# Kernel tuning notes

Measured on AMD Instinct MI355X. Metric: run time of the kernel, lower is better.

Reference implementation:

```python
import jax, jax.numpy as jnp
import numpy as np

N_NODES = 100_000
E_OFF = 1_500_000
LATENT = 64
MP_STEPS = 3


def setup_inputs() -> dict:
    key = jax.random.key(0)
    ks = jax.random.split(key, 12)
    # lower-triangular graph: all self-loops + random off-diagonal edges with row >= col
    r = jax.random.randint(ks[0], (E_OFF,), 0, N_NODES)
    c = jax.random.randint(ks[1], (E_OFF,), 0, N_NODES)
    diag = jnp.arange(N_NODES)
    edge_row = jnp.concatenate([jnp.maximum(r, c), diag]).astype(jnp.int64)
    edge_col = jnp.concatenate([jnp.minimum(r, c), diag]).astype(jnp.int64)
    E = E_OFF + N_NODES
    # positive weights (gcn_norm takes deg^{-1/2} of weighted degree)
    edge_attr = jax.random.uniform(ks[2], (E,), jnp.float32) + 0.05
    x = jax.random.normal(ks[3], (N_NODES, 1), jnp.float32)
    L = LATENT
    def lin(k, fi, fo):
        return jax.random.normal(k, (fi, fo), jnp.float32) / np.sqrt(fi)
    return {
        "x": x,
        "edge_attr": edge_attr,
        "w_enc": lin(ks[4], 1, L), "b_enc": jnp.zeros((L,), jnp.float32),
        "conv1_w": jax.random.normal(ks[5], (MP_STEPS, L, L), jnp.float32) / np.sqrt(L),
        "conv1_b": jnp.zeros((MP_STEPS, L), jnp.float32),
        "conv2_w": jax.random.normal(ks[6], (MP_STEPS, L, L), jnp.float32) / np.sqrt(L),
        "conv2_b": jnp.zeros((MP_STEPS, L), jnp.float32),
        "dec_w1": lin(ks[7], 2 * L, L), "dec_b1": jnp.zeros((L,), jnp.float32),
        "dec_w2": lin(ks[8], L, 1), "dec_b2": jnp.zeros((1,), jnp.float32),
        "edge_row": edge_row,
        "edge_col": edge_col,
    }


def reference(x, edge_attr, w_enc, b_enc, conv1_w, conv1_b, conv2_w, conv2_b,
              dec_w1, dec_b1, dec_w2, dec_b2, edge_row, edge_col):
    N = x.shape[0]
    # GCN normalization (graph already contains all self-loops, so PyG's
    # add_remaining_self_loops is a no-op and keeps existing loop weights)
    deg = jax.ops.segment_sum(edge_attr, edge_col, num_segments=N)
    dinv = jnp.where(deg > 0, jax.lax.rsqrt(jnp.maximum(deg, 1e-30)), 0.0)
    norm = dinv[edge_row] * edge_attr * dinv[edge_col]  # [E]
    cnt = jnp.maximum(
        jax.ops.segment_sum(jnp.ones_like(edge_attr), edge_col, num_segments=N), 1.0
    )[:, None]  # mean aggregation denominator

    def gcn(h, W, b):
        m = (h @ W)[edge_row] * norm[:, None]           # [E, F] messages
        agg = jax.ops.segment_sum(m, edge_col, num_segments=N) / cnt
        return agg + b

    # node encoder: single Linear (no activation)
    h = x @ w_enc + b_enc
    for i in range(MP_STEPS):
        h = jax.nn.relu(gcn(h, conv1_w[i], conv1_b[i]))
        h = jax.nn.relu(gcn(h, conv2_w[i], conv2_b[i]))

    # edge decoder: gather endpoints, MLP [2L -> L -> 1]
    e = jnp.concatenate([h[edge_row], h[edge_col]], axis=1)
    e = jax.nn.relu(e @ dec_w1 + dec_b1)
    e = (e @ dec_w2 + dec_b2)[:, 0]                      # [E]
    vals = jnp.where(edge_row == edge_col, jax.nn.softplus(e), e)
    return vals
```

## Files before the change

kernel.cpp:

```cpp
#include <hip/hip_runtime.h>
#include <hip/hip_fp16.h>
#include <math.h>

#define L 64
#define FIXS 1048576.0f
#define WAITCNT_LGKM0 0xC07F

static __device__ __forceinline__ __half2 h2add(__half2 a, __half2 b) {
    return __half2{__hadd(a.x, b.x), __hadd(a.y, b.y)};
}
static __device__ __forceinline__ __half2 h2relu(__half2 a) {
    const __half z = __float2half(0.f);
    return __half2{__hgt(a.x, z) ? a.x : z, __hgt(a.y, z) ? a.y : z};
}


__global__ void k_hist(const int* __restrict__ col, const float* __restrict__ attr,
                       unsigned long long* __restrict__ degcnt,
                       int* __restrict__ rank, int E) {
    int e = blockIdx.x * blockDim.x + threadIdx.x;
    if (e < E) {
        int c = col[e];
        unsigned int fx = (unsigned int)(int)rintf(attr[e] * FIXS);
        unsigned long long old = atomicAdd(&degcnt[c], (1ULL << 32) | (unsigned long long)fx);
        rank[e] = (int)(old >> 32);
    }
}

__global__ void k_dinv(const unsigned long long* __restrict__ degcnt,
                       float* __restrict__ dinv, int* __restrict__ cntI,
                       float* __restrict__ rcnt, int N) {
    int n = blockIdx.x * blockDim.x + threadIdx.x;
    if (n < N) {
        unsigned long long p = degcnt[n];
        int cnt = (int)(p >> 32);
        float d = (float)(unsigned int)(p & 0xffffffffULL) * (1.0f / FIXS);
        dinv[n] = (d > 0.f) ? (1.0f / sqrtf(fmaxf(d, 1e-30f))) : 0.f;
        cntI[n] = cnt;
        int c = cnt; if (c < 1) c = 1;
        rcnt[n] = 1.0f / (float)c;
    }
}


__global__ __launch_bounds__(256) void k_scan_a(const int* __restrict__ cntI,
                                                int* __restrict__ blockSums, int N) {
    __shared__ int red[4];
    int b = blockIdx.x, t = threadIdx.x;
    int base = b * 1024 + t * 4;
    int s = 0;
    #pragma unroll
    for (int i = 0; i < 4; ++i) { int idx = base + i; if (idx < N) s += cntI[idx]; }
    #pragma unroll
    for (int off = 32; off > 0; off >>= 1) s += __shfl_down(s, off);
    if ((t & 63) == 0) red[t >> 6] = s;
    __syncthreads();
    if (t == 0) blockSums[b] = red[0] + red[1] + red[2] + red[3];
}

__global__ __launch_bounds__(1024) void k_scan_b(int* __restrict__ blockSums, int B,
                                                 int* __restrict__ ptr, int N) {
    __shared__ int sh[1024];
    int t = threadIdx.x;
    sh[t] = (t < B) ? blockSums[t] : 0;
    __syncthreads();
    for (int off = 1; off < 1024; off <<= 1) {
        int v = (t >= off) ? sh[t - off] : 0;
        __syncthreads();
        sh[t] += v;
        __syncthreads();
    }
    if (t < B) blockSums[t] = (t == 0) ? 0 : sh[t - 1];
    if (t == B - 1) ptr[N] = sh[t];
}

__global__ __launch_bounds__(256) void k_scan_c(const int* __restrict__ cntI,
                                                const int* __restrict__ blockSums,
                                                int* __restrict__ ptr, int N) {
    __shared__ int th[256];
    int b = blockIdx.x, t = threadIdx.x;
    int base = b * 1024 + t * 4;
    int v[4]; int s = 0;
    #pragma unroll
    for (int i = 0; i < 4; ++i) {
        int idx = base + i;
        v[i] = (idx < N) ? cntI[idx] : 0;
        s += v[i];
    }
    th[t] = s;
    __syncthreads();
    for (int off = 1; off < 256; off <<= 1) {
        int x = (t >= off) ? th[t - off] : 0;
        __syncthreads();
        th[t] += x;
        __syncthreads();
    }
    int pre = ((t == 0) ? 0 : th[t - 1]) + blockSums[b];
    #pragma unroll
    for (int i = 0; i < 4; ++i) {
        int idx = base + i;
        if (idx < N) ptr[idx] = pre;
        pre += v[i];
    }
}

__global__ void k_scatter(const int* __restrict__ row, const int* __restrict__ col,
                          const float* __restrict__ attr, const float* __restrict__ dinv,
                          const int* __restrict__ colptr, const int* __restrict__ rank,
                          unsigned* __restrict__ csrX, int E) {
    int e = blockIdx.x * blockDim.x + threadIdx.x;
    if (e < E) {
        int r = row[e], c = col[e];
        float nrm = dinv[r] * attr[e] * dinv[c];
        unsigned short nb = __half_as_ushort(__float2half(nrm));
        csrX[colptr[c] + rank[e]] = (unsigned)r | ((unsigned)nb << 17);
    }
}


__global__ void k_encode(const float* __restrict__ x, const float* __restrict__ w_enc,
                         const float* __restrict__ b_enc, __half* __restrict__ h, int N) {
    int idx = blockIdx.x * blockDim.x + threadIdx.x;
    if (idx < N * L) {
        int n = idx >> 6, f = idx & 63;
        h[idx] = __float2half(x[n] * w_enc[f] + b_enc[f]);
    }
}


__global__ __launch_bounds__(256) void k_gcn(const uint2* __restrict__ h_in2,
        __half* __restrict__ h_out,
        const float* __restrict__ W, const float* __restrict__ bias,
        const int* __restrict__ colptr, const unsigned* __restrict__ csrX,
        const float* __restrict__ rcnt, int N) {
    __shared__ float sm[4][72];
    int lane = threadIdx.x & 63;
    int warp = threadIdx.x >> 6;
    int grp  = lane >> 4;
    int sub  = lane & 15;
    int wid  = (blockIdx.x * blockDim.x + threadIdx.x) >> 6;
    int nw   = (gridDim.x * blockDim.x) >> 6;
    float* smw = &sm[warp][0];

    float Wc[L];
    #pragma unroll
    for (int f = 0; f < L; ++f) Wc[f] = W[f * L + lane];
    float bl = bias[lane];

    for (int n = wid; n < N; n += nw) {
        int beg = colptr[n], end = colptr[n + 1];
        float4 sA = make_float4(0.f, 0.f, 0.f, 0.f);
        float4 sB = make_float4(0.f, 0.f, 0.f, 0.f);
        float4 sC = make_float4(0.f, 0.f, 0.f, 0.f);
        float4 sD = make_float4(0.f, 0.f, 0.f, 0.f);
        for (int base = beg; base < end; base += 64) {
            int m = end - base; if (m > 64) m = 64;
            unsigned mw = 0;
            if (lane < m) mw = csrX[base + lane];
            int kmax = (m + 3) >> 2;
            int k = 0;
            for (; k + 4 <= kmax; k += 4) {
                int j0 = 4 * k + grp;
                unsigned x0 = (unsigned)__shfl((int)mw, j0);
                unsigned x1 = (unsigned)__shfl((int)mw, j0 + 4);
                unsigned x2 = (unsigned)__shfl((int)mw, j0 + 8);
                unsigned x3 = (unsigned)__shfl((int)mw, j0 + 12);
                int r0 = (int)(x0 & 0x1FFFFu), r1 = (int)(x1 & 0x1FFFFu);
                int r2 = (int)(x2 & 0x1FFFFu), r3 = (int)(x3 & 0x1FFFFu);
                float w0 = __half2float(__ushort_as_half((unsigned short)(x0 >> 17)));
                float w1 = __half2float(__ushort_as_half((unsigned short)(x1 >> 17)));
                float w2 = __half2float(__ushort_as_half((unsigned short)(x2 >> 17)));
                float w3 = __half2float(__ushort_as_half((unsigned short)(x3 >> 17)));
                uint2 q0 = h_in2[(size_t)r0 * 16 + sub];
                uint2 q1 = h_in2[(size_t)r1 * 16 + sub];
                uint2 q2 = h_in2[(size_t)r2 * 16 + sub];
                uint2 q3 = h_in2[(size_t)r3 * 16 + sub];
                float2 l0 = __half22float2(*(__half2*)&q0.x), g0 = __half22float2(*(__half2*)&q0.y);
                float2 l1 = __half22float2(*(__half2*)&q1.x), g1 = __half22float2(*(__half2*)&q1.y);
                float2 l2 = __half22float2(*(__half2*)&q2.x), g2 = __half22float2(*(__half2*)&q2.y);
                float2 l3 = __half22float2(*(__half2*)&q3.x), g3 = __half22float2(*(__half2*)&q3.y);
                sA.x += w0 * l0.x; sA.y += w0 * l0.y; sA.z += w0 * g0.x; sA.w += w0 * g0.y;
                sB.x += w1 * l1.x; sB.y += w1 * l1.y; sB.z += w1 * g1.x; sB.w += w1 * g1.y;
                sC.x += w2 * l2.x; sC.y += w2 * l2.y; sC.z += w2 * g2.x; sC.w += w2 * g2.y;
                sD.x += w3 * l3.x; sD.y += w3 * l3.y; sD.z += w3 * g3.x; sD.w += w3 * g3.y;
            }
            for (; k < kmax; ++k) {
                int j0 = 4 * k + grp;
                unsigned x0 = (unsigned)__shfl((int)mw, j0);
                int   r0 = (int)(x0 & 0x1FFFFu);
                float w0 = __half2float(__ushort_as_half((unsigned short)(x0 >> 17)));
                uint2 q0 = h_in2[(size_t)r0 * 16 + sub];
                float2 l0 = __half22float2(*(__half2*)&q0.x), g0 = __half22float2(*(__half2*)&q0.y);
                sA.x += w0 * l0.x; sA.y += w0 * l0.y; sA.z += w0 * g0.x; sA.w += w0 * g0.y;
            }
        }
        float4 s;
        s.x = (sA.x + sB.x) + (sC.x + sD.x);
        s.y = (sA.y + sB.y) + (sC.y + sD.y);
        s.z = (sA.z + sB.z) + (sC.z + sD.z);
        s.w = (sA.w + sB.w) + (sC.w + sD.w);
        s.x += __shfl_xor(s.x, 16); s.x += __shfl_xor(s.x, 32);
        s.y += __shfl_xor(s.y, 16); s.y += __shfl_xor(s.y, 32);
        s.z += __shfl_xor(s.z, 16); s.z += __shfl_xor(s.z, 32);
        s.w += __shfl_xor(s.w, 16); s.w += __shfl_xor(s.w, 32);
        if (grp == 0) {
            smw[4 * sub + 0] = s.x; smw[4 * sub + 1] = s.y;
            smw[4 * sub + 2] = s.z; smw[4 * sub + 3] = s.w;
        }
        __builtin_amdgcn_s_waitcnt(WAITCNT_LGKM0);
        float a0 = 0.f, a1 = 0.f, a2 = 0.f, a3 = 0.f;
        const float4* smv = (const float4*)smw;
        #pragma unroll
        for (int q = 0; q < 16; ++q) {
            float4 sv = smv[q];
            a0 += sv.x * Wc[4 * q + 0];
            a1 += sv.y * Wc[4 * q + 1];
            a2 += sv.z * Wc[4 * q + 2];
            a3 += sv.w * Wc[4 * q + 3];
        }
        float o = ((a0 + a1) + (a2 + a3)) * rcnt[n] + bl;
        h_out[(size_t)n * L + lane] = __float2half(fmaxf(o, 0.f));
    }
}


__global__ __launch_bounds__(256) void k_mv2(const __half* __restrict__ h,
        const float* __restrict__ W1, const float* __restrict__ b1,
        __half* __restrict__ U, __half* __restrict__ V, int N) {
    __shared__ float sm[4][72];
    int lane = threadIdx.x & 63;
    int warp = threadIdx.x >> 6;
    int wid  = (blockIdx.x * blockDim.x + threadIdx.x) >> 6;
    int nw   = (gridDim.x * blockDim.x) >> 6;
    float* smw = &sm[warp][0];
    float Wu[L], Wv[L];
    #pragma unroll
    for (int f = 0; f < L; ++f) Wu[f] = W1[f * L + lane];
    #pragma unroll
    for (int f = 0; f < L; ++f) Wv[f] = W1[(L + f) * L + lane];
    float bl = b1[lane];
    for (int n = wid; n < N; n += nw) {
        float hl = __half2float(h[(size_t)n * L + lane]);
        smw[lane] = hl;
        __builtin_amdgcn_s_waitcnt(WAITCNT_LGKM0);
        float a0 = 0.f, a1 = 0.f, c0 = 0.f, c1 = 0.f;
        const float4* smv = (const float4*)smw;
        #pragma unroll
        for (int q = 0; q < 16; ++q) {
            float4 sv = smv[q];
            a0 += sv.x * Wu[4 * q + 0] ; a1 += sv.y * Wu[4 * q + 1];
            a0 += sv.z * Wu[4 * q + 2] ; a1 += sv.w * Wu[4 * q + 3];
            c0 += sv.x * Wv[4 * q + 0] ; c1 += sv.y * Wv[4 * q + 1];
            c0 += sv.z * Wv[4 * q + 2] ; c1 += sv.w * Wv[4 * q + 3];
        }
        U[(size_t)n * L + lane] = __float2half((a0 + a1) + bl);
        V[(size_t)n * L + lane] = __float2half(c0 + c1);
        __builtin_amdgcn_s_waitcnt(WAITCNT_LGKM0);
    }
}


__global__ __launch_bounds__(256) void k_edge(const __half* __restrict__ U,
        const __half* __restrict__ V, const float* __restrict__ w2,
        const float* __restrict__ b2,
        const int* __restrict__ colptr, const unsigned* __restrict__ csrX,
        float* __restrict__ tmp, int N) {
    int lane = threadIdx.x & 63;
    int half = lane & 1;
    int wid  = (blockIdx.x * blockDim.x + threadIdx.x) >> 6;
    int nw   = (gridDim.x * blockDim.x) >> 6;
    float w2f[32];
    #pragma unroll
    for (int k = 0; k < 32; ++k) w2f[k] = w2[32 * half + k];
    float b2v = b2[0];

    for (int n = wid; n < N; n += nw) {
        int beg = colptr[n], end = colptr[n + 1];
        const uint4* vrow = (const uint4*)(V + (size_t)n * L + 32 * half);
        uint4 v0 = vrow[0], v1 = vrow[1], v2 = vrow[2], v3 = vrow[3];
        for (int base = beg; base < end; base += 32) {
            int epos = base + (lane >> 1);
            if (epos < end) {
                unsigned md = csrX[epos];
                int r = (int)(md & 0x1FFFFu);
                const uint4* urow = (const uint4*)(U + (size_t)r * L + 32 * half);
                uint4 u0 = urow[0], u1 = urow[1], u2 = urow[2], u3 = urow[3];
                float p = 0.f;
                #define DOT8(uq, vq, B) { \
                    __half2 ta = h2relu(h2add(*(__half2*)&(uq).x, *(__half2*)&(vq).x)); \
                    __half2 tb = h2relu(h2add(*(__half2*)&(uq).y, *(__half2*)&(vq).y)); \
                    __half2 tc = h2relu(h2add(*(__half2*)&(uq).z, *(__half2*)&(vq).z)); \
                    __half2 td = h2relu(h2add(*(__half2*)&(uq).w, *(__half2*)&(vq).w)); \
                    float2 fa = __half22float2(ta), fb = __half22float2(tb); \
                    float2 fc = __half22float2(tc), fd = __half22float2(td); \
                    p += fa.x * w2f[B+0] + fa.y * w2f[B+1] + fb.x * w2f[B+2] + fb.y * w2f[B+3]; \
                    p += fc.x * w2f[B+4] + fc.y * w2f[B+5] + fd.x * w2f[B+6] + fd.y * w2f[B+7]; }
                DOT8(u0, v0, 0) DOT8(u1, v1, 8) DOT8(u2, v2, 16) DOT8(u3, v3, 24)
                #undef DOT8
                p += __shfl_xor(p, 1);
                if (half == 0) {
                    float val = p + b2v;
                    if (r == n) val = fmaxf(val, 0.f) + log1pf(expf(-fabsf(val)));
                    tmp[epos] = val;
                }
            }
        }
    }
}


__global__ void k_perm(const int* __restrict__ ecol, const int* __restrict__ rank,
                       const int* __restrict__ colptr, const float* __restrict__ tmp,
                       float* __restrict__ out, int E) {
    int e = blockIdx.x * blockDim.x + threadIdx.x;
    if (e < E) out[e] = tmp[colptr[ecol[e]] + rank[e]];
}


extern "C" void kernel_launch(void* const* d_in, const int* in_sizes, int n_in,
                              void* d_out, int out_size, void* d_ws, size_t ws_size,
                              hipStream_t stream) {
    const float* x     = (const float*)d_in[0];
    const float* attr  = (const float*)d_in[1];
    const float* w_enc = (const float*)d_in[2];
    const float* b_enc = (const float*)d_in[3];
    const float* c1w   = (const float*)d_in[4];
    const float* c1b   = (const float*)d_in[5];
    const float* c2w   = (const float*)d_in[6];
    const float* c2b   = (const float*)d_in[7];
    const float* dw1   = (const float*)d_in[8];
    const float* db1   = (const float*)d_in[9];
    const float* dw2   = (const float*)d_in[10];
    const float* db2   = (const float*)d_in[11];
    const int*   erow  = (const int*)d_in[12];
    const int*   ecol  = (const int*)d_in[13];
    int N = in_sizes[0];
    int E = in_sizes[1];
    float* out = (float*)d_out;

    char* w = (char*)d_ws;
    auto alloc = [&](size_t bytes) {
        char* p = w; w += (bytes + 255) & ~(size_t)255; return p;
    };
    unsigned long long* degcnt = (unsigned long long*)alloc((size_t)N * 8);
    size_t zbytes = (size_t)(w - (char*)d_ws);
    float* dinv   = (float*)alloc((size_t)N * 4);
    int*   cntI   = (int*)  alloc((size_t)N * 4);
    float* rcnt   = (float*)alloc((size_t)N * 4);
    int*   colptr = (int*)  alloc((size_t)(N + 1) * 4);
    int*   bsums  = (int*)  alloc(((size_t)(N + 1023) / 1024 + 1) * 4);
    int*   rank   = (int*)  alloc((size_t)E * 4);
    unsigned* csrX = (unsigned*)alloc((size_t)E * 4);
    float* tmp    = (float*)alloc((size_t)E * 4);
    __half* hA    = (__half*)alloc((size_t)N * L * 2);
    __half* hB    = (__half*)alloc((size_t)N * L * 2);
    __half* hU    = (__half*)alloc((size_t)N * L * 2);
    __half* hV    = (__half*)alloc((size_t)N * L * 2);
    (void)ws_size; (void)n_in; (void)out_size;

    (void)hipMemsetAsync(d_ws, 0, zbytes, stream);

    int eb = (E + 255) / 256;
    int nb = (N + 255) / 256;
    int B  = (N + 1023) / 1024;
    k_hist<<<eb, 256, 0, stream>>>(ecol, attr, degcnt, rank, E);
    k_dinv<<<nb, 256, 0, stream>>>(degcnt, dinv, cntI, rcnt, N);
    k_scan_a<<<B, 256, 0, stream>>>(cntI, bsums, N);
    k_scan_b<<<1, 1024, 0, stream>>>(bsums, B, colptr, N);
    k_scan_c<<<B, 256, 0, stream>>>(cntI, bsums, colptr, N);
    k_scatter<<<eb, 256, 0, stream>>>(erow, ecol, attr, dinv, colptr, rank, csrX, E);
    k_encode<<<(N * L + 255) / 256, 256, 0, stream>>>(x, w_enc, b_enc, hA, N);

    __half* hin = hA; __half* hout = hB;
    for (int i = 0; i < 3; ++i) {
        k_gcn<<<2048, 256, 0, stream>>>((const uint2*)hin, hout, c1w + i * L * L,
                                        c1b + i * L, colptr, csrX, rcnt, N);
        __half* t = hin; hin = hout; hout = t;
        k_gcn<<<2048, 256, 0, stream>>>((const uint2*)hin, hout, c2w + i * L * L,
                                        c2b + i * L, colptr, csrX, rcnt, N);
        t = hin; hin = hout; hout = t;
    }
    k_mv2<<<2048, 256, 0, stream>>>(hin, dw1, db1, hU, hV, N);
    k_edge<<<2048, 256, 0, stream>>>(hU, hV, dw2, db2, colptr, csrX, tmp, N);
    k_perm<<<eb, 256, 0, stream>>>(ecol, rank, colptr, tmp, out, E);
}
```

Measured before the change: 684.4 us.

## Privatize degree histogram per XCD and store final edge positions for permutation

The degree/count histogram is split into eight per-XCD copies, selected by reading the hardware XCD id register, so the 64-bit atomics can use workgroup scope and avoid cross-die coherence traffic. k_dinv reduces the copies and records per-XCD prefix offsets, which k_scatter uses to compute CSR positions. k_scatter then writes the final position back into rank, so k_perm needs one gather instead of two. The cost is an 8x larger zeroed histogram, an extra offset array, and more reads in k_dinv. Correctness depends on blocks only touching their own XCD copy, and workgroup-scope atomics across CUs on one XCD are a risky assumption.

Measured after the change: 691.1 us. No clear change (+1.0%).

```diff
diff --git a/kernel.cpp b/kernel.cpp
--- a/kernel.cpp
+++ b/kernel.cpp
@@ -4,6 +4,7 @@
 
 #define L 64
 #define FIXS 1048576.0f
+#define NXCD 8
 #define WAITCNT_LGKM0 0xC07F
 
 static __device__ __forceinline__ __half2 h2add(__half2 a, __half2 b) {
@@ -16,28 +17,41 @@
 
 
 __global__ void k_hist(const int* __restrict__ col, const float* __restrict__ attr,
-                       unsigned long long* __restrict__ degcnt,
-                       int* __restrict__ rank, int E) {
+                       unsigned long long* __restrict__ degcnt8,
+                       int* __restrict__ rank, int N, int E) {
+    unsigned xcd;
+    asm volatile("s_getreg_b32 %0, hwreg(20, 0, 32)" : "=s"(xcd));
+    xcd &= (NXCD - 1);
+    unsigned long long* base = degcnt8 + (size_t)xcd * (size_t)N;
     int e = blockIdx.x * blockDim.x + threadIdx.x;
     if (e < E) {
         int c = col[e];
         unsigned int fx = (unsigned int)(int)rintf(attr[e] * FIXS);
-        unsigned long long old = atomicAdd(&degcnt[c], (1ULL << 32) | (unsigned long long)fx);
-        rank[e] = (int)(old >> 32);
-    }
-}
-
-__global__ void k_dinv(const unsigned long long* __restrict__ degcnt,
+        unsigned long long inc = (1ULL << 32) | (unsigned long long)fx;
+        unsigned long long old = __hip_atomic_fetch_add(
+            &base[c], inc, __ATOMIC_RELAXED, __HIP_MEMORY_SCOPE_WORKGROUP);
+        rank[e] = (int)(((unsigned)(old >> 32) << 3) | xcd);
+    }
+}
+
+__global__ void k_dinv(const unsigned long long* __restrict__ degcnt8,
                        float* __restrict__ dinv, int* __restrict__ cntI,
-                       float* __restrict__ rcnt, int N) {
+                       float* __restrict__ rcnt,
+                       unsigned short* __restrict__ xcdoff, int N) {
     int n = blockIdx.x * blockDim.x + threadIdx.x;
     if (n < N) {
-        unsigned long long p = degcnt[n];
-        int cnt = (int)(p >> 32);
-        float d = (float)(unsigned int)(p & 0xffffffffULL) * (1.0f / FIXS);
+        unsigned cnt = 0, fxs = 0;
+        #pragma unroll
+        for (int x = 0; x < NXCD; ++x) {
+            unsigned long long p = degcnt8[(size_t)x * N + n];
+            xcdoff[(size_t)x * N + n] = (unsigned short)cnt;
+            cnt += (unsigned)(p >> 32);
+            fxs += (unsigned)(p & 0xffffffffULL);
+        }
+        float d = (float)fxs * (1.0f / FIXS);
         dinv[n] = (d > 0.f) ? (1.0f / sqrtf(fmaxf(d, 1e-30f))) : 0.f;
-        cntI[n] = cnt;
-        int c = cnt; if (c < 1) c = 1;
+        cntI[n] = (int)cnt;
+        unsigned c = cnt ? cnt : 1u;
         rcnt[n] = 1.0f / (float)c;
     }
 }
@@ -106,14 +120,21 @@
 
 __global__ void k_scatter(const int* __restrict__ row, const int* __restrict__ col,
                           const float* __restrict__ attr, const float* __restrict__ dinv,
-                          const int* __restrict__ colptr, const int* __restrict__ rank,
-                          unsigned* __restrict__ csrX, int E) {
+                          const int* __restrict__ colptr,
+                          const unsigned short* __restrict__ xcdoff,
+                          int* __restrict__ rank ,
+                          unsigned* __restrict__ csrX, int N, int E) {
     int e = blockIdx.x * blockDim.x + threadIdx.x;
     if (e < E) {
         int r = row[e], c = col[e];
+        int pk = rank[e];
+        int xcd = pk & (NXCD - 1);
+        int lr  = pk >> 3;
+        int pos = colptr[c] + (int)xcdoff[(size_t)xcd * N + c] + lr;
         float nrm = dinv[r] * attr[e] * dinv[c];
         unsigned short nb = __half_as_ushort(__float2half(nrm));
-        csrX[colptr[c] + rank[e]] = (unsigned)r | ((unsigned)nb << 17);
+        csrX[pos] = (unsigned)r | ((unsigned)nb << 17);
+        rank[e] = pos;
     }
 }
 
@@ -309,11 +330,10 @@
 }
 
 
-__global__ void k_perm(const int* __restrict__ ecol, const int* __restrict__ rank,
-                       const int* __restrict__ colptr, const float* __restrict__ tmp,
+__global__ void k_perm(const int* __restrict__ epos, const float* __restrict__ tmp,
                        float* __restrict__ out, int E) {
     int e = blockIdx.x * blockDim.x + threadIdx.x;
-    if (e < E) out[e] = tmp[colptr[ecol[e]] + rank[e]];
+    if (e < E) out[e] = tmp[epos[e]];
 }
 
 
@@ -342,11 +362,12 @@
     auto alloc = [&](size_t bytes) {
         char* p = w; w += (bytes + 255) & ~(size_t)255; return p;
     };
-    unsigned long long* degcnt = (unsigned long long*)alloc((size_t)N * 8);
+    unsigned long long* degcnt = (unsigned long long*)alloc((size_t)N * 8 * NXCD);
     size_t zbytes = (size_t)(w - (char*)d_ws);
     float* dinv   = (float*)alloc((size_t)N * 4);
     int*   cntI   = (int*)  alloc((size_t)N * 4);
     float* rcnt   = (float*)alloc((size_t)N * 4);
+    unsigned short* xcdoff = (unsigned short*)alloc((size_t)N * 2 * NXCD);
     int*   colptr = (int*)  alloc((size_t)(N + 1) * 4);
     int*   bsums  = (int*)  alloc(((size_t)(N + 1023) / 1024 + 1) * 4);
     int*   rank   = (int*)  alloc((size_t)E * 4);
@@ -363,12 +384,13 @@
     int eb = (E + 255) / 256;
     int nb = (N + 255) / 256;
     int B  = (N + 1023) / 1024;
-    k_hist<<<eb, 256, 0, stream>>>(ecol, attr, degcnt, rank, E);
-    k_dinv<<<nb, 256, 0, stream>>>(degcnt, dinv, cntI, rcnt, N);
+    k_hist<<<eb, 256, 0, stream>>>(ecol, attr, degcnt, rank, N, E);
+    k_dinv<<<nb, 256, 0, stream>>>(degcnt, dinv, cntI, rcnt, xcdoff, N);
     k_scan_a<<<B, 256, 0, stream>>>(cntI, bsums, N);
     k_scan_b<<<1, 1024, 0, stream>>>(bsums, B, colptr, N);
     k_scan_c<<<B, 256, 0, stream>>>(cntI, bsums, colptr, N);
-    k_scatter<<<eb, 256, 0, stream>>>(erow, ecol, attr, dinv, colptr, rank, csrX, E);
+    k_scatter<<<eb, 256, 0, stream>>>(erow, ecol, attr, dinv, colptr, xcdoff,
+                                      rank, csrX, N, E);
     k_encode<<<(N * L + 255) / 256, 256, 0, stream>>>(x, w_enc, b_enc, hA, N);
 
     __half* hin = hA; __half* hout = hB;
@@ -382,5 +404,5 @@
     }
     k_mv2<<<2048, 256, 0, stream>>>(hin, dw1, db1, hU, hV, N);
     k_edge<<<2048, 256, 0, stream>>>(hU, hV, dw2, db2, colptr, csrX, tmp, N);
-    k_perm<<<eb, 256, 0, stream>>>(ecol, rank, colptr, tmp, out, E);
-}
+    k_perm<<<eb, 256, 0, stream>>>(rank, tmp, out, E);
+}
```
